# Kernel tuning notes

Measured on AMD Instinct MI355X. Metric: run time of the kernel, lower is better.

## Reference

```python
import jax, jax.numpy as jnp
import numpy as np

N = 100000          # nodes
E = 1600000         # random edges (self loops appended in reference)
F_IN = 256          # dataset.num_features
NUM_CLASSES = 7     # dataset.num_classes
H = 2 * NUM_CLASSES # heads = 14
C = NUM_CLASSES     # per-head channels (concat=False)
NEG_SLOPE = 0.2     # GATConv default leaky_relu slope


def setup_inputs() -> dict:
    key = jax.random.key(0)
    ks = jax.random.split(key, 10)
    x = jax.random.normal(ks[0], (N, F_IN), jnp.float32)
    edge_index = jax.random.randint(ks[1], (2, E), 0, N, jnp.int32)
    def glorot(k, shape, fan_in):
        return jax.random.normal(k, shape, jnp.float32) * (1.0 / np.sqrt(fan_in))
    return {
        "x": x,
        "edge_index": edge_index,
        "W1": glorot(ks[2], (F_IN, H * C), F_IN),
        "a_src1": glorot(ks[3], (H, C), C),
        "a_dst1": glorot(ks[4], (H, C), C),
        "b1": jnp.zeros((C,), jnp.float32),
        "W2": glorot(ks[5], (C, H * C), C),
        "a_src2": glorot(ks[6], (H, C), C),
        "a_dst2": glorot(ks[7], (H, C), C),
        "b2": jnp.zeros((C,), jnp.float32),
    }


def gat_conv(x, src, dst, W, a_src, a_dst, b):
    # x: [N, Fin] -> per-head projections [N, H, C]
    xh = (x @ W).reshape(N, H, C)
    # per-node attention logits [N, H]
    al_src = jnp.einsum("nhc,hc->nh", xh, a_src)
    al_dst = jnp.einsum("nhc,hc->nh", xh, a_dst)
    # per-edge logits (message flows src -> dst)
    alpha = jax.nn.leaky_relu(al_src[src] + al_dst[dst], NEG_SLOPE)  # [E', H]
    # segment softmax over incoming edges of each destination node
    amax = jax.ops.segment_max(jax.lax.stop_gradient(alpha), dst, num_segments=N)
    alpha = jnp.exp(alpha - amax[dst])
    denom = jax.ops.segment_sum(alpha, dst, num_segments=N)
    alpha = alpha / denom[dst]
    # weighted messages, then MAX aggregation per destination (aggr='max')
    msg = alpha[:, :, None] * xh[src]                    # [E', H, C]
    out = jax.ops.segment_max(msg, dst, num_segments=N)  # [N, H, C]
    # concat=False -> mean over heads, plus bias
    return out.mean(axis=1) + b                          # [N, C]


def reference(x, edge_index, W1, a_src1, a_dst1, b1, W2, a_src2, a_dst2, b2):
    # GATConv(add_self_loops=True): append self loops so every node has >=1 in-edge
    loops = jnp.arange(N, dtype=edge_index.dtype)
    src = jnp.concatenate([edge_index[0], loops])
    dst = jnp.concatenate([edge_index[1], loops])
    h = gat_conv(x, src, dst, W1, a_src1, a_dst1, b1)
    h = jax.nn.relu(h)
    h = gat_conv(h, src, dst, W2, a_src2, a_dst2, b2)
    return jax.nn.log_softmax(h, axis=1)
```

## Files before the change

kernel.cpp:

```cpp
#include <hip/hip_runtime.h>
#include <math.h>

#define H  14
#define C  7
#define HC 98
#define FIN 256
#define NEG_SLOPE 0.2f
#define LOG2E 1.44269504088896f

#define BSHIFT 9
#define BSIZE  512
#define NBUCK_MAX 256

typedef __attribute__((ext_vector_type(8))) short short8;
typedef __attribute__((ext_vector_type(4))) float floatx4;
typedef _Float16 h2 __attribute__((ext_vector_type(2)));

#define WT_ROWS   112
#define WT_STRIDE 264
#define VS_STRIDE 99

__device__ __forceinline__ unsigned bf16r(float f) {
    unsigned u = __float_as_uint(f);
    return (u + 0x7FFFu + ((u >> 16) & 1u)) >> 16;
}

__device__ __forceinline__ h2 u2h(unsigned u) { return __builtin_bit_cast(h2, u); }
__device__ __forceinline__ unsigned hpk(float a, float b) {
    h2 v = { (_Float16)a, (_Float16)b };
    return __builtin_bit_cast(unsigned, v);
}
__device__ __forceinline__ float hhi(unsigned w) {
    unsigned short s = (unsigned short)(w >> 16);
    return (float)__builtin_bit_cast(_Float16, s);
}
__device__ __forceinline__ h2 hshfl_max(h2 v, int mask) {
    int u = __builtin_bit_cast(int, v);
    int o = __shfl_xor(u, mask, 64);
    return __builtin_elementwise_max(v, u2h((unsigned)o));
}


__global__ void k_zero(int* __restrict__ p, int n) {
    int i = blockIdx.x * blockDim.x + threadIdx.x;
    if (i < n) p[i] = 0;
}

__global__ __launch_bounds__(256) void k_hist(const int* __restrict__ ei, int E,
                                              int* __restrict__ gcnt, int nb) {
    __shared__ int hist[NBUCK_MAX];
    const int t = threadIdx.x;
    for (int i = t; i < nb; i += 256) hist[i] = 0;
    __syncthreads();
    const int stride = gridDim.x * 256;
    for (int e = blockIdx.x * 256 + t; e < E; e += stride)
        atomicAdd(&hist[ei[E + e] >> BSHIFT], 1);
    __syncthreads();
    for (int i = t; i < nb; i += 256)
        if (hist[i]) atomicAdd(gcnt + i, hist[i]);
}

__global__ __launch_bounds__(1024) void k_bscan(const int* __restrict__ gcnt,
                                                int* __restrict__ boff, int* __restrict__ bcur,
                                                int* __restrict__ row_ptr, int nb, int N) {
    __shared__ int sd[1024];
    int t = threadIdx.x;
    int own = (t < nb) ? gcnt[t] : 0;
    sd[t] = own;
    __syncthreads();
    #pragma unroll
    for (int off = 1; off < 1024; off <<= 1) {
        int v = (t >= off) ? sd[t - off] : 0;
        __syncthreads();
        sd[t] += v;
        __syncthreads();
    }
    if (t < nb) {
        boff[t + 1] = sd[t];
        bcur[t] = sd[t] - own;
        if (t == nb - 1) row_ptr[N] = sd[t];
    }
    if (t == 0) boff[0] = 0;
}

__global__ __launch_bounds__(256) void k_part(const int* __restrict__ ei, int E,
                                              int* __restrict__ bcur, int2* __restrict__ pedge,
                                              int nb) {
    __shared__ int hist[NBUCK_MAX];
    __shared__ int start[NBUCK_MAX];
    const int t = threadIdx.x;
    const int chunk = (E + gridDim.x - 1) / gridDim.x;
    const int c0 = blockIdx.x * chunk;
    const int c1 = min(c0 + chunk, E);
    for (int i = t; i < nb; i += 256) hist[i] = 0;
    __syncthreads();
    for (int e = c0 + t; e < c1; e += 256)
        atomicAdd(&hist[ei[E + e] >> BSHIFT], 1);
    __syncthreads();
    for (int i = t; i < nb; i += 256) {
        int h = hist[i];
        start[i] = h ? atomicAdd(bcur + i, h) : 0;
        hist[i] = 0;
    }
    __syncthreads();
    for (int e = c0 + t; e < c1; e += 256) {
        int s = ei[e], d = ei[E + e];
        int b = d >> BSHIFT;
        int pos = start[b] + atomicAdd(&hist[b], 1);
        pedge[pos] = make_int2(s, d);
    }
}

__global__ __launch_bounds__(512) void k_bcsr(const int2* __restrict__ pedge,
                                              const int* __restrict__ boff,
                                              int* __restrict__ row_ptr, int* __restrict__ col,
                                              int N) {
    __shared__ int cnt[BSIZE];
    __shared__ int sc[BSIZE];
    __shared__ int cur[BSIZE];
    const int b  = blockIdx.x;
    const int t  = threadIdx.x;
    const int e0 = boff[b], e1 = boff[b + 1];
    const int base = b << BSHIFT;
    const int nv = min(BSIZE, N - base);
    cnt[t] = 0;
    __syncthreads();
    for (int e = e0 + t; e < e1; e += 512)
        atomicAdd(&cnt[pedge[e].y - base], 1);
    __syncthreads();
    sc[t] = cnt[t];
    __syncthreads();
    #pragma unroll
    for (int off = 1; off < BSIZE; off <<= 1) {
        int v = (t >= off) ? sc[t - off] : 0;
        __syncthreads();
        sc[t] += v;
        __syncthreads();
    }
    if (t < nv) {
        int excl = sc[t] - cnt[t];
        row_ptr[base + t] = e0 + excl;
        cur[t] = excl;
    }
    __syncthreads();
    for (int e = e0 + t; e < e1; e += 512) {
        int2 r = pedge[e];
        int d = r.y - base;
        int pos = e0 + atomicAdd(&cur[d], 1);
        col[pos] = r.x;
    }
}


__global__ void k_convW(const float* __restrict__ W, unsigned short* __restrict__ WtG) {
    int id = blockIdx.x * blockDim.x + threadIdx.x;
    int n = id >> 8, k = id & 255;
    float v = (n < HC) ? W[k * HC + n] : 0.f;
    WtG[id] = (unsigned short)(__float_as_uint(v) >> 16);
}

__global__ __launch_bounds__(256) void k_proj1_mfma(
    const float* __restrict__ x, const unsigned short* __restrict__ WtG,
    const float* __restrict__ asrc, const float* __restrict__ adst,
    uint4* __restrict__ xpack, float* __restrict__ aldst, int N)
{
    __shared__ unsigned short wt_s[WT_ROWS * WT_STRIDE];
    __shared__ float as_s[HC], ad_s[HC];
    float* vals_s = (float*)wt_s;
    const int t  = threadIdx.x;
    const int wv = t >> 6;
    const int l  = t & 63;
    const int ln = l & 15;
    const int qd = l >> 4;
    const int rowBase = blockIdx.x * 64;

    #pragma unroll
    for (int i = 0; i < 14; ++i) {
        int f = i * 256 + t;
        int r = f >> 5, pos = f & 31;
        *(uint4*)(wt_s + r * WT_STRIDE + pos * 8) = ((const uint4*)WtG)[f];
    }
    if (t < HC) { as_s[t] = asrc[t]; ad_s[t] = adst[t]; }
    __syncthreads();

    int gr = rowBase + (wv << 4) + ln; if (gr >= N) gr = N - 1;
    const float* xr = x + (size_t)gr * FIN;

    short8 afr[8];
    #pragma unroll
    for (int s = 0; s < 8; ++s) {
        float4 v0 = *(const float4*)(xr + s * 32 + qd * 8);
        float4 v1 = *(const float4*)(xr + s * 32 + qd * 8 + 4);
        short8 a;
        a[0] = (short)(__float_as_uint(v0.x) >> 16);
        a[1] = (short)(__float_as_uint(v0.y) >> 16);
        a[2] = (short)(__float_as_uint(v0.z) >> 16);
        a[3] = (short)(__float_as_uint(v0.w) >> 16);
        a[4] = (short)(__float_as_uint(v1.x) >> 16);
        a[5] = (short)(__float_as_uint(v1.y) >> 16);
        a[6] = (short)(__float_as_uint(v1.z) >> 16);
        a[7] = (short)(__float_as_uint(v1.w) >> 16);
        afr[s] = a;
    }

    floatx4 acc[7] = {};
    #pragma unroll
    for (int s = 0; s < 8; ++s) {
        const int k0 = s * 32;
        #pragma unroll
        for (int ct = 0; ct < 7; ++ct) {
            short8 b = *(const short8*)(wt_s + (ct * 16 + ln) * WT_STRIDE + k0 + qd * 8);
            acc[ct] = __builtin_amdgcn_mfma_f32_16x16x32_bf16(afr[s], b, acc[ct], 0, 0, 0);
        }
    }

    __syncthreads();
    #pragma unroll
    for (int ct = 0; ct < 7; ++ct) {
        int colg = ct * 16 + ln;
        if (colg < HC) {
            #pragma unroll
            for (int r = 0; r < 4; ++r)
                vals_s[((wv << 4) + (qd << 2) + r) * VS_STRIDE + colg] = acc[ct][r];
        }
    }
    __syncthreads();

    for (int p = t; p < 64 * H; p += 256) {
        int nl = p / H, h = p - nl * H;
        int gn = rowBase + nl;
        if (gn >= N) break;
        const float* vp = vals_s + nl * VS_STRIDE + h * C;
        float v[C];
        float s1 = 0.f, s2 = 0.f;
        #pragma unroll
        for (int c2 = 0; c2 < C; ++c2) {
            float f = vp[c2];
            v[c2] = f;
            s1 = fmaf(f, as_s[h * C + c2], s1);
            s2 = fmaf(f, ad_s[h * C + c2], s2);
        }
        uint4 pk;
        pk.x = hpk(v[0], v[1]);
        pk.y = hpk(v[2], v[3]);
        pk.z = hpk(v[4], v[5]);
        pk.w = hpk(v[6], s1 * LOG2E);
        xpack[(size_t)gn * H + h] = pk;
        aldst[(size_t)gn * H + h] = s2 * LOG2E;
    }
}


__global__ __launch_bounds__(256) void k_proj2_pack(
    const float* __restrict__ h1, const float* __restrict__ W,
    const float* __restrict__ asrc, const float* __restrict__ adst,
    uint4* __restrict__ xpack, float* __restrict__ aldst, int N)
{
    __shared__ float Ws[C * HC];
    __shared__ float as_s[HC], ad_s[HC];
    const int t = threadIdx.x;
    for (int i = t; i < C * HC; i += 256) Ws[i] = W[i];
    if (t < HC) { as_s[t] = asrc[t]; ad_s[t] = adst[t]; }
    __syncthreads();
    int n = blockIdx.x * 256 + t;
    if (n >= N) return;
    float xr[C];
    #pragma unroll
    for (int c2 = 0; c2 < C; ++c2) xr[c2] = h1[(size_t)n * C + c2];
    #pragma unroll
    for (int h = 0; h < H; ++h) {
        float v[C], s1 = 0.f, s2 = 0.f;
        #pragma unroll
        for (int c2 = 0; c2 < C; ++c2) {
            float acc = 0.f;
            #pragma unroll
            for (int k = 0; k < C; ++k)
                acc = fmaf(xr[k], Ws[k * HC + h * C + c2], acc);
            v[c2] = acc;
            s1 = fmaf(acc, as_s[h * C + c2], s1);
            s2 = fmaf(acc, ad_s[h * C + c2], s2);
        }
        uint4 pk;
        pk.x = hpk(v[0], v[1]);
        pk.y = hpk(v[2], v[3]);
        pk.z = hpk(v[4], v[5]);
        pk.w = hpk(v[6], s1 * LOG2E);
        xpack[(size_t)n * H + h] = pk;
        aldst[(size_t)n * H + h] = s2 * LOG2E;
    }
}

#define AGG_STEP(DEN, REC)                                              \
    {                                                                   \
        float l = hhi((REC).w) + ld;                                    \
        float p = __builtin_amdgcn_exp2f(fmaxf(l, 0.2f * l) - K);       \
        DEN += p;                                                       \
        _Float16 ph = (_Float16)p;                                      \
        h2 p2 = { ph, ph };                                             \
        m0 = __builtin_elementwise_max(m0, p2 * u2h((REC).x));          \
        m1 = __builtin_elementwise_max(m1, p2 * u2h((REC).y));          \
        m2 = __builtin_elementwise_max(m2, p2 * u2h((REC).z));          \
        m3 = __builtin_elementwise_max(m3, p2 * u2h((REC).w));          \
    }

template<int LAYER>
__global__ __launch_bounds__(256) void k_agg(
    const int* __restrict__ row_ptr, const int* __restrict__ col,
    const uint4* __restrict__ xpack, const float* __restrict__ aldst,
    const float* __restrict__ bias,
    float* __restrict__ h1, float* __restrict__ out, int N)
{
    const int t    = threadIdx.x;
    const int lane = t & 63;
    const int e4   = lane >> 4;
    const int h    = lane & 15;
    const int n    = blockIdx.x * 4 + (t >> 6);
    const bool act = (h < H) && (n < N);

    float den = 0.f, den2 = 0.f;
    h2 m0 = u2h(0xFC00FC00u), m1 = m0, m2 = m0, m3 = m0;
    float ld = 0.f, K = 0.f;

    if (act) {
        const int e0  = row_ptr[n];
        const int deg = row_ptr[n + 1] - e0;
        ld = aldst[(size_t)n * H + h];
        float kb = ld + 2.0f * LOG2E;
        K = fmaxf(kb, 0.2f * kb);

        if (e4 == 0) {
            uint4 pk = xpack[(size_t)n * H + h];
            float l = hhi(pk.w) + ld;
            float p = __builtin_amdgcn_exp2f(fmaxf(l, 0.2f * l) - K);
            den = p;
            _Float16 ph = (_Float16)p;
            h2 p2 = { ph, ph };
            m0 = p2 * u2h(pk.x);
            m1 = p2 * u2h(pk.y);
            m2 = p2 * u2h(pk.z);
            m3 = p2 * u2h(pk.w);
        }

        if (deg > 0) {
            const int last = deg - 1;
            int i = e4;
            int c0 = col[e0 + min(i,      last)];
            int c1 = col[e0 + min(i + 4,  last)];
            uint4 r0 = xpack[(size_t)c0 * H + h];
            uint4 r1 = xpack[(size_t)c1 * H + h];
            c0 = col[e0 + min(i + 8,  last)];
            c1 = col[e0 + min(i + 12, last)];
            for (; i < deg; i += 8) {
                uint4 curA = r0, curB = r1;
                r0 = xpack[(size_t)c0 * H + h];
                r1 = xpack[(size_t)c1 * H + h];
                c0 = col[e0 + min(i + 16, last)];
                c1 = col[e0 + min(i + 20, last)];
                AGG_STEP(den,  curA);
                if (i + 4 < deg) AGG_STEP(den2, curB);
            }
        }
    }
    den += den2;

    den += __shfl_xor(den, 16, 64);
    den += __shfl_xor(den, 32, 64);
    m0 = hshfl_max(m0, 16); m0 = hshfl_max(m0, 32);
    m1 = hshfl_max(m1, 16); m1 = hshfl_max(m1, 32);
    m2 = hshfl_max(m2, 16); m2 = hshfl_max(m2, 32);
    m3 = hshfl_max(m3, 16); m3 = hshfl_max(m3, 32);

    float v[C];
    if (act) {
        float rd = 1.f / den;
        v[0] = (float)m0.x * rd; v[1] = (float)m0.y * rd;
        v[2] = (float)m1.x * rd; v[3] = (float)m1.y * rd;
        v[4] = (float)m2.x * rd; v[5] = (float)m2.y * rd;
        v[6] = (float)m3.x * rd;
    } else {
        #pragma unroll
        for (int c = 0; c < C; ++c) v[c] = 0.f;
    }

    #pragma unroll
    for (int off = 1; off <= 8; off <<= 1) {
        #pragma unroll
        for (int c = 0; c < C; ++c) v[c] += __shfl_xor(v[c], off, 64);
    }

    if (n >= N) return;
    if (LAYER == 1) {
        if (lane < C) {
            float myv = v[0];
            #pragma unroll
            for (int c = 1; c < C; ++c) if (lane == c) myv = v[c];
            h1[(size_t)n * C + lane] = fmaxf(myv * (1.f / H) + bias[lane], 0.f);
        }
    } else {
        float o[C];
        #pragma unroll
        for (int c = 0; c < C; ++c) o[c] = v[c] * (1.f / H) + bias[c];
        float mv = o[0];
        #pragma unroll
        for (int c = 1; c < C; ++c) mv = fmaxf(mv, o[c]);
        float lse = 0.f;
        #pragma unroll
        for (int c = 0; c < C; ++c) lse += __expf(o[c] - mv);
        lse = logf(lse);
        if (lane < C) {
            float myo = o[0];
            #pragma unroll
            for (int c = 1; c < C; ++c) if (lane == c) myo = o[c];
            out[(size_t)n * C + lane] = myo - mv - lse;
        }
    }
}


static inline size_t align16(size_t v) { return (v + 15) & ~(size_t)15; }

extern "C" void kernel_launch(void* const* d_in, const int* in_sizes, int n_in,
                              void* d_out, int out_size, void* d_ws, size_t ws_size,
                              hipStream_t stream)
{
    const float* x     = (const float*)d_in[0];
    const int*   ei    = (const int*)d_in[1];
    const float* W1    = (const float*)d_in[2];
    const float* asrc1 = (const float*)d_in[3];
    const float* adst1 = (const float*)d_in[4];
    const float* b1    = (const float*)d_in[5];
    const float* W2    = (const float*)d_in[6];
    const float* asrc2 = (const float*)d_in[7];
    const float* adst2 = (const float*)d_in[8];
    const float* b2    = (const float*)d_in[9];

    const int N  = in_sizes[0] / FIN;
    const int E  = in_sizes[1] / 2;
    const int nb = (N + BSIZE - 1) >> BSHIFT;

    char* w = (char*)d_ws;
    uint4* xpack   = (uint4*)w; w += align16((size_t)N * H * 16);
    int2*  pedge   = (int2*)w;  w += align16((size_t)E * 8);
    float* aldst   = (float*)w; w += align16((size_t)N * H * 4);
    float* h1      = (float*)w; w += align16((size_t)N * C * 4);
    int*   row_ptr = (int*)w;   w += align16((size_t)(N + 1) * 4);
    int*   col     = (int*)w;   w += align16((size_t)E * 4);
    int*   gcnt    = (int*)w;   w += align16((size_t)nb * 4);
    int*   boff    = (int*)w;   w += align16((size_t)(nb + 1) * 4);
    int*   bcur    = (int*)w;   w += align16((size_t)nb * 4);
    unsigned short* WtG = (unsigned short*)w; w += align16((size_t)WT_ROWS * FIN * 2);

    const int gAgg  = (N + 3) / 4;
    const int gMfma = (N + 63) / 64;
    const int g256N = (N + 255) / 256;

    k_zero<<<1, 256, 0, stream>>>(gcnt, nb);
    k_hist<<<256, 256, 0, stream>>>(ei, E, gcnt, nb);
    k_bscan<<<1, 1024, 0, stream>>>(gcnt, boff, bcur, row_ptr, nb, N);
    k_part<<<256, 256, 0, stream>>>(ei, E, bcur, pedge, nb);
    k_bcsr<<<nb, 512, 0, stream>>>(pedge, boff, row_ptr, col, N);

    k_convW<<<(WT_ROWS * FIN + 255) / 256, 256, 0, stream>>>(W1, WtG);
    k_proj1_mfma<<<gMfma, 256, 0, stream>>>(x, WtG, asrc1, adst1, xpack, aldst, N);
    k_agg<1><<<gAgg, 256, 0, stream>>>(row_ptr, col, xpack, aldst, b1,
                                       h1, (float*)d_out, N);
    k_proj2_pack<<<g256N, 256, 0, stream>>>(h1, W2, asrc2, adst2, xpack, aldst, N);
    k_agg<2><<<gAgg, 256, 0, stream>>>(row_ptr, col, xpack, aldst, b2,
                                       h1, (float*)d_out, N);
}
```

Before: 409.0 us.

## Build CSR via per-node degree atomics instead of two-pass bucket partition

Replaces the bucket-partition CSR construction (histogram, partition into a pedge buffer, per-bucket local sort) with global per-node degree atomics, a per-bucket scan to produce row_ptr, and a fill pass that scatters sources using global atomic cursors. This removes the intermediate int2 edge buffer and one full pass over the edges, at the cost of many contended global atomics. Because the fill is atomic, neighbor order within a row becomes nondeterministic, which is harmless for the max and sum aggregation. The aggregation kernel also drops the clamped index reads by padding col with zeros and prefetching past the row end, and it switches index arithmetic to 32-bit unsigned.

```diff
diff --git a/kernel.cpp b/kernel.cpp
--- a/kernel.cpp
+++ b/kernel.cpp
@@ -20,11 +20,6 @@
 #define WT_STRIDE 264
 #define VS_STRIDE 99
 
-__device__ __forceinline__ unsigned bf16r(float f) {
-    unsigned u = __float_as_uint(f);
-    return (u + 0x7FFFu + ((u >> 16) & 1u)) >> 16;
-}
-
 __device__ __forceinline__ h2 u2h(unsigned u) { return __builtin_bit_cast(h2, u); }
 __device__ __forceinline__ unsigned hpk(float a, float b) {
     h2 v = { (_Float16)a, (_Float16)b };
@@ -41,27 +36,26 @@
 }
 
 
-__global__ void k_zero(int* __restrict__ p, int n) {
-    int i = blockIdx.x * blockDim.x + threadIdx.x;
-    if (i < n) p[i] = 0;
-}
-
-__global__ __launch_bounds__(256) void k_hist(const int* __restrict__ ei, int E,
-                                              int* __restrict__ gcnt, int nb) {
+__global__ __launch_bounds__(256) void k_deg(const int* __restrict__ ei, int E,
+                                             int* __restrict__ deg,
+                                             int* __restrict__ gcnt, int nb) {
     __shared__ int hist[NBUCK_MAX];
     const int t = threadIdx.x;
     for (int i = t; i < nb; i += 256) hist[i] = 0;
     __syncthreads();
     const int stride = gridDim.x * 256;
-    for (int e = blockIdx.x * 256 + t; e < E; e += stride)
-        atomicAdd(&hist[ei[E + e] >> BSHIFT], 1);
+    for (int e = blockIdx.x * 256 + t; e < E; e += stride) {
+        int d = ei[E + e];
+        atomicAdd(deg + d, 1);
+        atomicAdd(&hist[d >> BSHIFT], 1);
+    }
     __syncthreads();
     for (int i = t; i < nb; i += 256)
         if (hist[i]) atomicAdd(gcnt + i, hist[i]);
 }
 
 __global__ __launch_bounds__(1024) void k_bscan(const int* __restrict__ gcnt,
-                                                int* __restrict__ boff, int* __restrict__ bcur,
+                                                int* __restrict__ boff,
                                                 int* __restrict__ row_ptr, int nb, int N) {
     __shared__ int sd[1024];
     int t = threadIdx.x;
@@ -77,58 +71,22 @@
     }
     if (t < nb) {
         boff[t + 1] = sd[t];
-        bcur[t] = sd[t] - own;
         if (t == nb - 1) row_ptr[N] = sd[t];
     }
     if (t == 0) boff[0] = 0;
 }
 
-__global__ __launch_bounds__(256) void k_part(const int* __restrict__ ei, int E,
-                                              int* __restrict__ bcur, int2* __restrict__ pedge,
-                                              int nb) {
-    __shared__ int hist[NBUCK_MAX];
-    __shared__ int start[NBUCK_MAX];
+__global__ __launch_bounds__(512) void k_rowptr(const int* __restrict__ deg,
+                                                const int* __restrict__ boff,
+                                                int* __restrict__ row_ptr,
+                                                int* __restrict__ cur, int N) {
+    __shared__ int sc[BSIZE];
+    const int b = blockIdx.x;
     const int t = threadIdx.x;
-    const int chunk = (E + gridDim.x - 1) / gridDim.x;
-    const int c0 = blockIdx.x * chunk;
-    const int c1 = min(c0 + chunk, E);
-    for (int i = t; i < nb; i += 256) hist[i] = 0;
-    __syncthreads();
-    for (int e = c0 + t; e < c1; e += 256)
-        atomicAdd(&hist[ei[E + e] >> BSHIFT], 1);
-    __syncthreads();
-    for (int i = t; i < nb; i += 256) {
-        int h = hist[i];
-        start[i] = h ? atomicAdd(bcur + i, h) : 0;
-        hist[i] = 0;
-    }
-    __syncthreads();
-    for (int e = c0 + t; e < c1; e += 256) {
-        int s = ei[e], d = ei[E + e];
-        int b = d >> BSHIFT;
-        int pos = start[b] + atomicAdd(&hist[b], 1);
-        pedge[pos] = make_int2(s, d);
-    }
-}
-
-__global__ __launch_bounds__(512) void k_bcsr(const int2* __restrict__ pedge,
-                                              const int* __restrict__ boff,
-                                              int* __restrict__ row_ptr, int* __restrict__ col,
-                                              int N) {
-    __shared__ int cnt[BSIZE];
-    __shared__ int sc[BSIZE];
-    __shared__ int cur[BSIZE];
-    const int b  = blockIdx.x;
-    const int t  = threadIdx.x;
-    const int e0 = boff[b], e1 = boff[b + 1];
     const int base = b << BSHIFT;
     const int nv = min(BSIZE, N - base);
-    cnt[t] = 0;
-    __syncthreads();
-    for (int e = e0 + t; e < e1; e += 512)
-        atomicAdd(&cnt[pedge[e].y - base], 1);
-    __syncthreads();
-    sc[t] = cnt[t];
+    int d = (t < nv) ? deg[base + t] : 0;
+    sc[t] = d;
     __syncthreads();
     #pragma unroll
     for (int off = 1; off < BSIZE; off <<= 1) {
@@ -138,16 +96,19 @@
         __syncthreads();
     }
     if (t < nv) {
-        int excl = sc[t] - cnt[t];
-        row_ptr[base + t] = e0 + excl;
-        cur[t] = excl;
-    }
-    __syncthreads();
-    for (int e = e0 + t; e < e1; e += 512) {
-        int2 r = pedge[e];
-        int d = r.y - base;
-        int pos = e0 + atomicAdd(&cur[d], 1);
-        col[pos] = r.x;
+        int rp = boff[b] + sc[t] - d;
+        row_ptr[base + t] = rp;
+        cur[base + t] = rp;
+    }
+}
+
+__global__ __launch_bounds__(256) void k_fill(const int* __restrict__ ei, int E,
+                                              int* __restrict__ cur, int* __restrict__ col) {
+    const int stride = gridDim.x * 256;
+    for (int e = blockIdx.x * 256 + threadIdx.x; e < E; e += stride) {
+        int s = ei[e], d = ei[E + e];
+        int pos = atomicAdd(cur + d, 1);
+        col[pos] = s;
     }
 }
 
@@ -324,12 +285,12 @@
     if (act) {
         const int e0  = row_ptr[n];
         const int deg = row_ptr[n + 1] - e0;
-        ld = aldst[(size_t)n * H + h];
+        ld = aldst[(unsigned)n * H + h];
         float kb = ld + 2.0f * LOG2E;
         K = fmaxf(kb, 0.2f * kb);
 
         if (e4 == 0) {
-            uint4 pk = xpack[(size_t)n * H + h];
+            uint4 pk = xpack[(unsigned)n * H + h];
             float l = hhi(pk.w) + ld;
             float p = __builtin_amdgcn_exp2f(fmaxf(l, 0.2f * l) - K);
             den = p;
@@ -342,20 +303,20 @@
         }
 
         if (deg > 0) {
-            const int last = deg - 1;
+            const int* cp = col + e0;
             int i = e4;
-            int c0 = col[e0 + min(i,      last)];
-            int c1 = col[e0 + min(i + 4,  last)];
-            uint4 r0 = xpack[(size_t)c0 * H + h];
-            uint4 r1 = xpack[(size_t)c1 * H + h];
-            c0 = col[e0 + min(i + 8,  last)];
-            c1 = col[e0 + min(i + 12, last)];
+            int c0 = cp[i];
+            int c1 = cp[i + 4];
+            uint4 r0 = xpack[(unsigned)c0 * H + h];
+            uint4 r1 = xpack[(unsigned)c1 * H + h];
+            c0 = cp[i + 8];
+            c1 = cp[i + 12];
             for (; i < deg; i += 8) {
                 uint4 curA = r0, curB = r1;
-                r0 = xpack[(size_t)c0 * H + h];
-                r1 = xpack[(size_t)c1 * H + h];
-                c0 = col[e0 + min(i + 16, last)];
-                c1 = col[e0 + min(i + 20, last)];
+                r0 = xpack[(unsigned)c0 * H + h];
+                r1 = xpack[(unsigned)c1 * H + h];
+                c0 = cp[i + 16];
+                c1 = cp[i + 20];
                 AGG_STEP(den,  curA);
                 if (i + 4 < deg) AGG_STEP(den2, curB);
             }
@@ -440,25 +401,26 @@
 
     char* w = (char*)d_ws;
     uint4* xpack   = (uint4*)w; w += align16((size_t)N * H * 16);
-    int2*  pedge   = (int2*)w;  w += align16((size_t)E * 8);
     float* aldst   = (float*)w; w += align16((size_t)N * H * 4);
     float* h1      = (float*)w; w += align16((size_t)N * C * 4);
     int*   row_ptr = (int*)w;   w += align16((size_t)(N + 1) * 4);
-    int*   col     = (int*)w;   w += align16((size_t)E * 4);
-    int*   gcnt    = (int*)w;   w += align16((size_t)nb * 4);
+    int*   col     = (int*)w;   w += align16((size_t)(E + 64) * 4);
+    int*   deg     = (int*)w;   w += align16((size_t)(N + nb) * 4);
+    int*   cur     = (int*)w;   w += align16((size_t)N * 4);
     int*   boff    = (int*)w;   w += align16((size_t)(nb + 1) * 4);
-    int*   bcur    = (int*)w;   w += align16((size_t)nb * 4);
     unsigned short* WtG = (unsigned short*)w; w += align16((size_t)WT_ROWS * FIN * 2);
+    int* gcnt = deg + N;
 
     const int gAgg  = (N + 3) / 4;
     const int gMfma = (N + 63) / 64;
     const int g256N = (N + 255) / 256;
 
-    k_zero<<<1, 256, 0, stream>>>(gcnt, nb);
-    k_hist<<<256, 256, 0, stream>>>(ei, E, gcnt, nb);
-    k_bscan<<<1, 1024, 0, stream>>>(gcnt, boff, bcur, row_ptr, nb, N);
-    k_part<<<256, 256, 0, stream>>>(ei, E, bcur, pedge, nb);
-    k_bcsr<<<nb, 512, 0, stream>>>(pedge, boff, row_ptr, col, N);
+    hipMemsetAsync(deg, 0, (size_t)(N + nb) * 4, stream);
+    hipMemsetAsync(col + E, 0, 64 * 4, stream);
+    k_deg<<<256, 256, 0, stream>>>(ei, E, deg, gcnt, nb);
+    k_bscan<<<1, 1024, 0, stream>>>(gcnt, boff, row_ptr, nb, N);
+    k_rowptr<<<nb, 512, 0, stream>>>(deg, boff, row_ptr, cur, N);
+    k_fill<<<256, 256, 0, stream>>>(ei, E, cur, col);
 
     k_convW<<<(WT_ROWS * FIN + 255) / 256, 256, 0, stream>>>(W1, WtG);
     k_proj1_mfma<<<gMfma, 256, 0, stream>>>(x, WtG, asrc1, adst1, xpack, aldst, N);
```

Result: slower. 506.1 us (+23.7%).

## Read MFMA weights directly from global memory and drop clamped column indexing

Applied to the files above, without the earlier changes.

The projection kernel stops staging the bf16 weight matrix in LDS and loads B fragments straight from global memory (relying on cache), which removes a barrier and lets the 64-row vals buffer use its own smaller shared allocation. The aggregation kernel drops the min() clamps on CSR column reads by padding the col array with 64 zeroed entries, so prefetch reads past the end stay in bounds and point at node 0. Index arithmetic switches from size_t to unsigned. These cut LDS traffic and ALU work, at the cost of more global and L2 traffic for the weights, and the padding only protects the last node's row while other rows' speculative prefetches read neighbouring rows.

```diff
diff --git a/kernel.cpp b/kernel.cpp
--- a/kernel.cpp
+++ b/kernel.cpp
@@ -17,13 +17,7 @@
 typedef _Float16 h2 __attribute__((ext_vector_type(2)));
 
 #define WT_ROWS   112
-#define WT_STRIDE 264
 #define VS_STRIDE 99
-
-__device__ __forceinline__ unsigned bf16r(float f) {
-    unsigned u = __float_as_uint(f);
-    return (u + 0x7FFFu + ((u >> 16) & 1u)) >> 16;
-}
 
 __device__ __forceinline__ h2 u2h(unsigned u) { return __builtin_bit_cast(h2, u); }
 __device__ __forceinline__ unsigned hpk(float a, float b) {
@@ -41,9 +35,10 @@
 }
 
 
-__global__ void k_zero(int* __restrict__ p, int n) {
+__global__ void k_zero2(int* __restrict__ a, int na, int* __restrict__ b, int nbb) {
     int i = blockIdx.x * blockDim.x + threadIdx.x;
-    if (i < n) p[i] = 0;
+    if (i < na) a[i] = 0;
+    if (i < nbb) b[i] = 0;
 }
 
 __global__ __launch_bounds__(256) void k_hist(const int* __restrict__ ei, int E,
@@ -164,9 +159,8 @@
     const float* __restrict__ asrc, const float* __restrict__ adst,
     uint4* __restrict__ xpack, float* __restrict__ aldst, int N)
 {
-    __shared__ unsigned short wt_s[WT_ROWS * WT_STRIDE];
+    __shared__ float vals_s[64 * VS_STRIDE];
     __shared__ float as_s[HC], ad_s[HC];
-    float* vals_s = (float*)wt_s;
     const int t  = threadIdx.x;
     const int wv = t >> 6;
     const int l  = t & 63;
@@ -174,14 +168,7 @@
     const int qd = l >> 4;
     const int rowBase = blockIdx.x * 64;
 
-    #pragma unroll
-    for (int i = 0; i < 14; ++i) {
-        int f = i * 256 + t;
-        int r = f >> 5, pos = f & 31;
-        *(uint4*)(wt_s + r * WT_STRIDE + pos * 8) = ((const uint4*)WtG)[f];
-    }
     if (t < HC) { as_s[t] = asrc[t]; ad_s[t] = adst[t]; }
-    __syncthreads();
 
     int gr = rowBase + (wv << 4) + ln; if (gr >= N) gr = N - 1;
     const float* xr = x + (size_t)gr * FIN;
@@ -203,18 +190,18 @@
         afr[s] = a;
     }
 
+    const unsigned short* wb = WtG + ln * 256 + qd * 8;
+
     floatx4 acc[7] = {};
     #pragma unroll
     for (int s = 0; s < 8; ++s) {
-        const int k0 = s * 32;
         #pragma unroll
         for (int ct = 0; ct < 7; ++ct) {
-            short8 b = *(const short8*)(wt_s + (ct * 16 + ln) * WT_STRIDE + k0 + qd * 8);
+            short8 b = *(const short8*)(wb + ct * (16 * 256) + s * 32);
             acc[ct] = __builtin_amdgcn_mfma_f32_16x16x32_bf16(afr[s], b, acc[ct], 0, 0, 0);
         }
     }
 
-    __syncthreads();
     #pragma unroll
     for (int ct = 0; ct < 7; ++ct) {
         int colg = ct * 16 + ln;
@@ -324,12 +311,12 @@
     if (act) {
         const int e0  = row_ptr[n];
         const int deg = row_ptr[n + 1] - e0;
-        ld = aldst[(size_t)n * H + h];
+        ld = aldst[(unsigned)n * H + h];
         float kb = ld + 2.0f * LOG2E;
         K = fmaxf(kb, 0.2f * kb);
 
         if (e4 == 0) {
-            uint4 pk = xpack[(size_t)n * H + h];
+            uint4 pk = xpack[(unsigned)n * H + h];
             float l = hhi(pk.w) + ld;
             float p = __builtin_amdgcn_exp2f(fmaxf(l, 0.2f * l) - K);
             den = p;
@@ -342,20 +329,20 @@
         }
 
         if (deg > 0) {
-            const int last = deg - 1;
+            const int* cp = col + e0;
             int i = e4;
-            int c0 = col[e0 + min(i,      last)];
-            int c1 = col[e0 + min(i + 4,  last)];
-            uint4 r0 = xpack[(size_t)c0 * H + h];
-            uint4 r1 = xpack[(size_t)c1 * H + h];
-            c0 = col[e0 + min(i + 8,  last)];
-            c1 = col[e0 + min(i + 12, last)];
+            int c0 = cp[i];
+            int c1 = cp[i + 4];
+            uint4 r0 = xpack[(unsigned)c0 * H + h];
+            uint4 r1 = xpack[(unsigned)c1 * H + h];
+            c0 = cp[i + 8];
+            c1 = cp[i + 12];
             for (; i < deg; i += 8) {
                 uint4 curA = r0, curB = r1;
-                r0 = xpack[(size_t)c0 * H + h];
-                r1 = xpack[(size_t)c1 * H + h];
-                c0 = col[e0 + min(i + 16, last)];
-                c1 = col[e0 + min(i + 20, last)];
+                r0 = xpack[(unsigned)c0 * H + h];
+                r1 = xpack[(unsigned)c1 * H + h];
+                c0 = cp[i + 16];
+                c1 = cp[i + 20];
                 AGG_STEP(den,  curA);
                 if (i + 4 < deg) AGG_STEP(den2, curB);
             }
@@ -444,7 +431,7 @@
     float* aldst   = (float*)w; w += align16((size_t)N * H * 4);
     float* h1      = (float*)w; w += align16((size_t)N * C * 4);
     int*   row_ptr = (int*)w;   w += align16((size_t)(N + 1) * 4);
-    int*   col     = (int*)w;   w += align16((size_t)E * 4);
+    int*   col     = (int*)w;   w += align16((size_t)(E + 64) * 4);
     int*   gcnt    = (int*)w;   w += align16((size_t)nb * 4);
     int*   boff    = (int*)w;   w += align16((size_t)(nb + 1) * 4);
     int*   bcur    = (int*)w;   w += align16((size_t)nb * 4);
@@ -454,7 +441,7 @@
     const int gMfma = (N + 63) / 64;
     const int g256N = (N + 255) / 256;
 
-    k_zero<<<1, 256, 0, stream>>>(gcnt, nb);
+    k_zero2<<<1, 256, 0, stream>>>(gcnt, nb, col + E, 64);
     k_hist<<<256, 256, 0, stream>>>(ei, E, gcnt, nb);
     k_bscan<<<1, 1024, 0, stream>>>(gcnt, boff, bcur, row_ptr, nb, N);
     k_part<<<256, 256, 0, stream>>>(ei, E, bcur, pedge, nb);
```

New measurement: 457.2 us. 1.12x slower.
